# Kernel optimization log

Hardware: AMD Instinct MI355X
Metric: run time of the kernel (lower is better)

Reference implementation:

```python
import jax, jax.numpy as jnp
import numpy as np

N = 50000
E = 800000
IN_DIM = 128
HID = 64
HEADS = 4
OUT_DIM = 64
NEG_SLOPE = 0.2


def setup_inputs() -> dict:
    key = jax.random.key(0)
    ks = jax.random.split(key, 10)
    x = jax.random.normal(ks[0], (N, IN_DIM), dtype=jnp.float32)
    edge_index = jax.random.randint(ks[1], (2, E), 0, N, dtype=jnp.int64)
    s1 = 1.0 / np.sqrt(IN_DIM)
    s2 = 1.0 / np.sqrt(HEADS * HID)
    return {
        "x": x,
        "edge_index": edge_index,
        "W1": jax.random.normal(ks[2], (IN_DIM, HEADS * HID), dtype=jnp.float32) * s1,
        "a_src1": jax.random.normal(ks[3], (HEADS, HID), dtype=jnp.float32) * s2,
        "a_dst1": jax.random.normal(ks[4], (HEADS, HID), dtype=jnp.float32) * s2,
        "b1": jnp.zeros((HEADS * HID,), dtype=jnp.float32),
        "W2": jax.random.normal(ks[5], (HEADS * HID, OUT_DIM), dtype=jnp.float32) * s2,
        "a_src2": jax.random.normal(ks[6], (1, OUT_DIM), dtype=jnp.float32) * 0.125,
        "a_dst2": jax.random.normal(ks[7], (1, OUT_DIM), dtype=jnp.float32) * 0.125,
        "b2": jnp.zeros((OUT_DIM,), dtype=jnp.float32),
    }


def gat_layer(x, src, dst, W, a_src, a_dst, bias, heads, ch, concat):
    n = x.shape[0]
    h = (x @ W).reshape(n, heads, ch)                      # [N,H,C]
    asrc = jnp.einsum('nhc,hc->nh', h, a_src)              # [N,H]
    adst = jnp.einsum('nhc,hc->nh', h, a_dst)              # [N,H]
    e = asrc[src] + adst[dst]                              # [E',H]
    e = jnp.where(e > 0, e, NEG_SLOPE * e)                 # LeakyReLU(0.2)
    # segment softmax over incoming edges of each dst node
    m = jax.ops.segment_max(e, dst, num_segments=n)        # [N,H]
    m = jnp.where(jnp.isfinite(m), m, 0.0)
    ex = jnp.exp(e - m[dst])
    denom = jax.ops.segment_sum(ex, dst, num_segments=n)   # [N,H]
    alpha = ex / (denom[dst] + 1e-16)                      # [E',H]
    out = jax.ops.segment_sum(alpha[:, :, None] * h[src], dst, num_segments=n)  # [N,H,C]
    if concat:
        out = out.reshape(n, heads * ch)
    else:
        out = out.mean(axis=1)
    return out + bias


def reference(x, edge_index, W1, a_src1, a_dst1, b1, W2, a_src2, a_dst2, b2):
    n = x.shape[0]
    loops = jnp.arange(n, dtype=edge_index.dtype)
    src = jnp.concatenate([edge_index[0], loops])          # add self-loops (PyG default)
    dst = jnp.concatenate([edge_index[1], loops])
    h = gat_layer(x, src, dst, W1, a_src1, a_dst1, b1, HEADS, HID, True)
    h = jax.nn.elu(h)
    out = gat_layer(h, src, dst, W2, a_src2, a_dst2, b2, 1, OUT_DIM, False)
    return out
```

## Files before the change

### kernel.cpp

```cpp
#include <hip/hip_runtime.h>
#include <hip/hip_bf16.h>

#define NN 50000
#define EE 800000
#define IN_DIM 128
#define HH 256
#define HID 64
#define HEADS 4
#define OUT_DIM 64
#define SCAN_BLOCKS 196
#define G1_BLOCKS 782
#define AGG_BLOCKS 3125
#define TOTW (AGG_BLOCKS * 4)

static __device__ __forceinline__ unsigned short f2bf(float f) {
    unsigned int u = __float_as_uint(f);
    u += 0x7fffu + ((u >> 16) & 1u);
    return (unsigned short)(u >> 16);
}
static __device__ __forceinline__ float bf2f(unsigned short h) {
    return __uint_as_float(((unsigned int)h) << 16);
}


__global__ void hist_kernel(const int* __restrict__ ei, int* __restrict__ deg) {
    int e = blockIdx.x * 256 + threadIdx.x;
    atomicAdd(&deg[ei[EE + e]], 1);
}

__global__ __launch_bounds__(256) void block_scan_kernel(
    const int* __restrict__ deg, int* __restrict__ local_scan,
    int* __restrict__ block_sum) {
    __shared__ int tmp[256];
    int t = threadIdx.x, i = blockIdx.x * 256 + t;
    int v = (i < NN) ? deg[i] : 0;
    tmp[t] = v;
    __syncthreads();
    for (int d = 1; d < 256; d <<= 1) {
        int u = (t >= d) ? tmp[t - d] : 0;
        __syncthreads();
        tmp[t] += u;
        __syncthreads();
    }
    if (i < NN) local_scan[i] = tmp[t] - v;
    if (t == 255) block_sum[blockIdx.x] = tmp[255];
}

__global__ __launch_bounds__(256) void scan_sums_kernel(int* __restrict__ block_sum) {
    __shared__ int tmp[256];
    int t = threadIdx.x;
    int v = (t < SCAN_BLOCKS) ? block_sum[t] : 0;
    tmp[t] = v;
    __syncthreads();
    for (int d = 1; d < 256; d <<= 1) {
        int u = (t >= d) ? tmp[t - d] : 0;
        __syncthreads();
        tmp[t] += u;
        __syncthreads();
    }
    if (t < SCAN_BLOCKS) block_sum[t] = tmp[t] - v;
}

__global__ __launch_bounds__(256) void finalize_kernel(
    const int* __restrict__ local_scan, const int* __restrict__ block_sum,
    int* __restrict__ row_ptr, int* __restrict__ cursor) {
    int i = blockIdx.x * 256 + threadIdx.x;
    if (i < NN) {
        int v = local_scan[i] + block_sum[blockIdx.x];
        row_ptr[i] = v; cursor[i] = v;
    }
    if (i == 0) row_ptr[NN] = EE;
}

__global__ void scatter_kernel(const int* __restrict__ ei, int* __restrict__ cursor,
                               int* __restrict__ edge_src) {
    int e = blockIdx.x * 256 + threadIdx.x;
    int d = ei[EE + e];
    int pos = atomicAdd(&cursor[d], 1);
    edge_src[pos] = ei[e];
}


__global__ __launch_bounds__(256) void gemm1_kernel(
    const float* __restrict__ x, const float* __restrict__ W1,
    const float* __restrict__ a_src1, const float* __restrict__ a_dst1,
    unsigned short* __restrict__ h1, float* __restrict__ asrc1, float* __restrict__ adst1) {
    __shared__ __align__(16) float xs[64][IN_DIM];
    int t = threadIdx.x;
    int row0 = blockIdx.x * 64;
    #pragma unroll
    for (int j = 0; j < 8; j++) {
        int idx = t + j * 256;
        int r = idx >> 5, k4 = (idx & 31) * 4;
        int rr = row0 + r; if (rr >= NN) rr = NN - 1;
        *reinterpret_cast<float4*>(&xs[r][k4]) =
            *reinterpret_cast<const float4*>(&x[(size_t)rr * IN_DIM + k4]);
    }
    __syncthreads();
    int lane = t & 63, wid = t >> 6;
    float4 acc[16];
    #pragma unroll
    for (int r = 0; r < 16; r++) acc[r] = make_float4(0.f, 0.f, 0.f, 0.f);
    const float* wbase = W1 + lane * 4;
    float4 w0 = *reinterpret_cast<const float4*>(&wbase[0 * HH]);
    float4 w1 = *reinterpret_cast<const float4*>(&wbase[1 * HH]);
    float4 w2 = *reinterpret_cast<const float4*>(&wbase[2 * HH]);
    float4 w3 = *reinterpret_cast<const float4*>(&wbase[3 * HH]);
    for (int k = 0; k < IN_DIM; k += 4) {
        int kn = (k + 4) & 127;
        float4 nw0 = *reinterpret_cast<const float4*>(&wbase[(kn + 0) * HH]);
        float4 nw1 = *reinterpret_cast<const float4*>(&wbase[(kn + 1) * HH]);
        float4 nw2 = *reinterpret_cast<const float4*>(&wbase[(kn + 2) * HH]);
        float4 nw3 = *reinterpret_cast<const float4*>(&wbase[(kn + 3) * HH]);
        #pragma unroll
        for (int r = 0; r < 16; r++) {
            float4 xv = *reinterpret_cast<const float4*>(&xs[wid * 16 + r][k]);
            acc[r].x = fmaf(xv.x, w0.x, acc[r].x); acc[r].y = fmaf(xv.x, w0.y, acc[r].y);
            acc[r].z = fmaf(xv.x, w0.z, acc[r].z); acc[r].w = fmaf(xv.x, w0.w, acc[r].w);
            acc[r].x = fmaf(xv.y, w1.x, acc[r].x); acc[r].y = fmaf(xv.y, w1.y, acc[r].y);
            acc[r].z = fmaf(xv.y, w1.z, acc[r].z); acc[r].w = fmaf(xv.y, w1.w, acc[r].w);
            acc[r].x = fmaf(xv.z, w2.x, acc[r].x); acc[r].y = fmaf(xv.z, w2.y, acc[r].y);
            acc[r].z = fmaf(xv.z, w2.z, acc[r].z); acc[r].w = fmaf(xv.z, w2.w, acc[r].w);
            acc[r].x = fmaf(xv.w, w3.x, acc[r].x); acc[r].y = fmaf(xv.w, w3.y, acc[r].y);
            acc[r].z = fmaf(xv.w, w3.z, acc[r].z); acc[r].w = fmaf(xv.w, w3.w, acc[r].w);
        }
        w0 = nw0; w1 = nw1; w2 = nw2; w3 = nw3;
    }
    float4 asv = *reinterpret_cast<const float4*>(&a_src1[lane * 4]);
    float4 adv = *reinterpret_cast<const float4*>(&a_dst1[lane * 4]);
    int head = lane >> 4;
    #pragma unroll
    for (int r = 0; r < 16; r++) {
        int row = row0 + wid * 16 + r;
        bool ok = row < NN;
        if (ok) {
            ushort4 hv;
            hv.x = f2bf(acc[r].x); hv.y = f2bf(acc[r].y);
            hv.z = f2bf(acc[r].z); hv.w = f2bf(acc[r].w);
            *reinterpret_cast<ushort4*>(&h1[(size_t)row * HH + lane * 4]) = hv;
        }
        float vs = acc[r].x * asv.x + acc[r].y * asv.y + acc[r].z * asv.z + acc[r].w * asv.w;
        float vd = acc[r].x * adv.x + acc[r].y * adv.y + acc[r].z * adv.z + acc[r].w * adv.w;
        #pragma unroll
        for (int o = 1; o < 16; o <<= 1) { vs += __shfl_xor(vs, o); vd += __shfl_xor(vd, o); }
        if (ok && (lane & 15) == 0) {
            asrc1[row * HEADS + head] = vs;
            adst1[row * HEADS + head] = vd;
        }
    }
}


__global__ __launch_bounds__(256) void agg1_kernel(
    const int* __restrict__ row_ptr, const int* __restrict__ edge_src,
    const unsigned short* __restrict__ h1, const float* __restrict__ asrc1,
    const float* __restrict__ adst1, const float* __restrict__ b1,
    unsigned short* __restrict__ x2) {
    int wid = threadIdx.x >> 6, lane = threadIdx.x & 63;
    int gw = blockIdx.x * 4 + wid;
    int head = lane >> 4;
    unsigned cb = lane * 4;
    const unsigned short* h1l = h1 + cb;
    const float* asl = asrc1 + head;
    float4 bv = *reinterpret_cast<const float4*>(&b1[cb]);
    for (int node = gw; node < NN; node += TOTW) {
        float ad = adst1[node * HEADS + head];
        int beg = row_ptr[node], end = row_ptr[node + 1];
        float denom = 0.f;
        float ax = 0.f, ay = 0.f, az = 0.f, aw = 0.f;
        int s0 = (beg < end) ? edge_src[beg] : node;
        int s1 = (beg + 1 < end) ? edge_src[beg + 1] : node;
        int s2 = (beg + 2 < end) ? edge_src[beg + 2] : node;
        float e0 = asl[(unsigned)s0 * HEADS];
        float e1 = asl[(unsigned)s1 * HEADS];
        float e2 = asl[(unsigned)s2 * HEADS];
        ushort4 h0 = *reinterpret_cast<const ushort4*>(&h1l[(unsigned)s0 * HH]);
        ushort4 h1v = *reinterpret_cast<const ushort4*>(&h1l[(unsigned)s1 * HH]);
        ushort4 h2v = *reinterpret_cast<const ushort4*>(&h1l[(unsigned)s2 * HH]);
        for (int i = beg; i <= end; i++) {
            int j = i + 3;
            int s3 = (j < end) ? edge_src[j] : node;
            float e3 = asl[(unsigned)s3 * HEADS];
            ushort4 h3 = *reinterpret_cast<const ushort4*>(&h1l[(unsigned)s3 * HH]);
            float e = e0 + ad;
            e = fmaxf(e, 0.2f * e);
            float ex = __expf(e);
            denom += ex;
            ax = fmaf(ex, bf2f(h0.x), ax); ay = fmaf(ex, bf2f(h0.y), ay);
            az = fmaf(ex, bf2f(h0.z), az); aw = fmaf(ex, bf2f(h0.w), aw);
            e0 = e1; h0 = h1v;
            e1 = e2; h1v = h2v;
            e2 = e3; h2v = h3;
        }
        float inv = 1.0f / (denom + 1e-16f);
        float v0 = ax * inv + bv.x;
        float v1 = ay * inv + bv.y;
        float v2 = az * inv + bv.z;
        float v3 = aw * inv + bv.w;
        v0 = v0 > 0.f ? v0 : (__expf(v0) - 1.f);
        v1 = v1 > 0.f ? v1 : (__expf(v1) - 1.f);
        v2 = v2 > 0.f ? v2 : (__expf(v2) - 1.f);
        v3 = v3 > 0.f ? v3 : (__expf(v3) - 1.f);
        ushort4 o;
        o.x = f2bf(v0); o.y = f2bf(v1); o.z = f2bf(v2); o.w = f2bf(v3);
        *reinterpret_cast<ushort4*>(&x2[(size_t)node * HH + cb]) = o;
    }
}


__global__ __launch_bounds__(256) void gemm2_kernel(
    const unsigned short* __restrict__ x2, const float* __restrict__ W2,
    const float* __restrict__ a_src2, const float* __restrict__ a_dst2,
    unsigned short* __restrict__ h2, float* __restrict__ asrc2, float* __restrict__ adst2) {
    __shared__ __align__(16) float xs[32][HH];
    int t = threadIdx.x;
    int row0 = blockIdx.x * 32;
    #pragma unroll
    for (int j = 0; j < 8; j++) {
        int idx = t + j * 256;
        int r = idx >> 6, k4 = (idx & 63) * 4;
        int rr = row0 + r; if (rr >= NN) rr = NN - 1;
        ushort4 uv = *reinterpret_cast<const ushort4*>(&x2[(size_t)rr * HH + k4]);
        float4 fv;
        fv.x = bf2f(uv.x); fv.y = bf2f(uv.y); fv.z = bf2f(uv.z); fv.w = bf2f(uv.w);
        *reinterpret_cast<float4*>(&xs[r][k4]) = fv;
    }
    __syncthreads();
    int c = t & 63, wid = t >> 6;
    float acc[8];
    #pragma unroll
    for (int r = 0; r < 8; r++) acc[r] = 0.f;
    const float* wbase = W2 + c;
    float w0 = wbase[0 * OUT_DIM];
    float w1 = wbase[1 * OUT_DIM];
    float w2 = wbase[2 * OUT_DIM];
    float w3 = wbase[3 * OUT_DIM];
    for (int k = 0; k < HH; k += 4) {
        int kn = (k + 4) & 255;
        float nw0 = wbase[(kn + 0) * OUT_DIM];
        float nw1 = wbase[(kn + 1) * OUT_DIM];
        float nw2 = wbase[(kn + 2) * OUT_DIM];
        float nw3 = wbase[(kn + 3) * OUT_DIM];
        #pragma unroll
        for (int r = 0; r < 8; r++) {
            float4 xv = *reinterpret_cast<const float4*>(&xs[wid * 8 + r][k]);
            acc[r] = fmaf(xv.x, w0, acc[r]);
            acc[r] = fmaf(xv.y, w1, acc[r]);
            acc[r] = fmaf(xv.z, w2, acc[r]);
            acc[r] = fmaf(xv.w, w3, acc[r]);
        }
        w0 = nw0; w1 = nw1; w2 = nw2; w3 = nw3;
    }
    float as = a_src2[c], ad = a_dst2[c];
    #pragma unroll
    for (int r = 0; r < 8; r++) {
        int row = row0 + wid * 8 + r;
        bool ok = row < NN;
        if (ok) h2[(size_t)row * OUT_DIM + c] = f2bf(acc[r]);
        float vs = acc[r] * as, vd = acc[r] * ad;
        #pragma unroll
        for (int o = 32; o > 0; o >>= 1) { vs += __shfl_xor(vs, o); vd += __shfl_xor(vd, o); }
        if (ok && c == 0) { asrc2[row] = vs; adst2[row] = vd; }
    }
}


__global__ __launch_bounds__(256) void agg2_kernel(
    const int* __restrict__ row_ptr, const int* __restrict__ edge_src,
    const unsigned short* __restrict__ h2, const float* __restrict__ asrc2,
    const float* __restrict__ adst2, const float* __restrict__ b2,
    float* __restrict__ out) {
    int wid = threadIdx.x >> 6, lane = threadIdx.x & 63;
    int gw = blockIdx.x * 4 + wid;
    const unsigned short* h2l = h2 + lane;
    float bl = b2[lane];
    for (int node = gw; node < NN; node += TOTW) {
        float ad = adst2[node];
        int beg = row_ptr[node], end = row_ptr[node + 1];
        float denom = 0.f, acc = 0.f;
        int s0 = (beg < end) ? edge_src[beg] : node;
        int s1 = (beg + 1 < end) ? edge_src[beg + 1] : node;
        int s2 = (beg + 2 < end) ? edge_src[beg + 2] : node;
        float e0 = asrc2[s0], e1 = asrc2[s1], e2 = asrc2[s2];
        unsigned short h0 = h2l[(unsigned)s0 * OUT_DIM];
        unsigned short h1v = h2l[(unsigned)s1 * OUT_DIM];
        unsigned short h2v = h2l[(unsigned)s2 * OUT_DIM];
        for (int i = beg; i <= end; i++) {
            int j = i + 3;
            int s3 = (j < end) ? edge_src[j] : node;
            float e3 = asrc2[s3];
            unsigned short h3 = h2l[(unsigned)s3 * OUT_DIM];
            float e = e0 + ad;
            e = fmaxf(e, 0.2f * e);
            float ex = __expf(e);
            denom += ex;
            acc = fmaf(ex, bf2f(h0), acc);
            e0 = e1; h0 = h1v;
            e1 = e2; h1v = h2v;
            e2 = e3; h2v = h3;
        }
        out[(size_t)node * OUT_DIM + lane] = acc / (denom + 1e-16f) + bl;
    }
}


extern "C" void kernel_launch(void* const* d_in, const int* in_sizes, int n_in,
                              void* d_out, int out_size, void* d_ws, size_t ws_size,
                              hipStream_t stream) {
    const float* x   = (const float*)d_in[0];
    const int*   ei  = (const int*)d_in[1];
    const float* W1  = (const float*)d_in[2];
    const float* as1 = (const float*)d_in[3];
    const float* ad1 = (const float*)d_in[4];
    const float* b1  = (const float*)d_in[5];
    const float* W2  = (const float*)d_in[6];
    const float* as2 = (const float*)d_in[7];
    const float* ad2 = (const float*)d_in[8];
    const float* b2  = (const float*)d_in[9];
    float* out = (float*)d_out;

    char* ws = (char*)d_ws;
    size_t off = 0;
    auto alloc = [&](size_t bytes) -> void* {
        void* p = ws + off;
        off += (bytes + 255) & ~(size_t)255;
        return p;
    };
    unsigned short* h1 = (unsigned short*)alloc((size_t)NN * HH * 2);
    unsigned short* x2 = (unsigned short*)alloc((size_t)NN * HH * 2);
    unsigned short* h2 = (unsigned short*)alloc((size_t)NN * OUT_DIM * 2);
    float* asrc1  = (float*)alloc((size_t)NN * HEADS * 4);
    float* adst1  = (float*)alloc((size_t)NN * HEADS * 4);
    float* asrc2  = (float*)alloc((size_t)NN * 4);
    float* adst2  = (float*)alloc((size_t)NN * 4);
    int*   deg    = (int*)alloc((size_t)NN * 4);
    int*   row_ptr= (int*)alloc((size_t)(NN + 1) * 4);
    int*   cursor = (int*)alloc((size_t)NN * 4);
    int*   edge_src=(int*)alloc((size_t)EE * 4);
    int*   local_scan = (int*)alloc((size_t)NN * 4);
    int*   block_sum  = (int*)alloc((size_t)SCAN_BLOCKS * 4);

    hipMemsetAsync(deg, 0, (size_t)NN * 4, stream);
    hist_kernel<<<EE / 256, 256, 0, stream>>>(ei, deg);
    block_scan_kernel<<<SCAN_BLOCKS, 256, 0, stream>>>(deg, local_scan, block_sum);
    scan_sums_kernel<<<1, 256, 0, stream>>>(block_sum);
    finalize_kernel<<<SCAN_BLOCKS, 256, 0, stream>>>(local_scan, block_sum, row_ptr, cursor);
    gemm1_kernel<<<G1_BLOCKS, 256, 0, stream>>>(x, W1, as1, ad1, h1, asrc1, adst1);
    scatter_kernel<<<EE / 256, 256, 0, stream>>>(ei, cursor, edge_src);

    agg1_kernel<<<AGG_BLOCKS, 256, 0, stream>>>(row_ptr, edge_src, h1, asrc1, adst1, b1, x2);
    gemm2_kernel<<<(NN + 31) / 32, 256, 0, stream>>>(x2, W2, as2, ad2, h2, asrc2, adst2);
    agg2_kernel<<<AGG_BLOCKS, 256, 0, stream>>>(row_ptr, edge_src, h2, asrc2, adst2, b2, out);
}
```

Baseline: 418.1 us.

## Use bf16 MFMA for layer-1 GEMM and fold attention vectors into W1

Replaces the FP32 FMA layer-1 GEMM with a bf16 MFMA 16x16x32 kernel that reads a bf16 copy of x and a transposed bf16 W1. The per-head attention logits are now computed in a separate conversion pass as x·(W1·a) using a precomputed 128x8 projection, so the GEMM kernel only writes h1. This adds a single-block prep kernel and an extra pass over x, plus bf16 rounding of the inputs. The gemm2 weight prefetch is also simplified to direct loads.

After: 454.6 us. 8.7% more time.

```diff
diff --git a/kernel.cpp b/kernel.cpp
--- a/kernel.cpp
+++ b/kernel.cpp
@@ -9,7 +9,9 @@
 #define HEADS 4
 #define OUT_DIM 64
 #define SCAN_BLOCKS 196
-#define G1_BLOCKS 782
+#define G1M_BLOCKS 782
+#define XCVT_BLOCKS 1563
+#define XCVT_TOTW (XCVT_BLOCKS * 4)
 #define AGG_BLOCKS 3125
 #define TOTW (AGG_BLOCKS * 4)
 
@@ -21,6 +23,9 @@
 static __device__ __forceinline__ float bf2f(unsigned short h) {
     return __uint_as_float(((unsigned int)h) << 16);
 }
+
+typedef __attribute__((ext_vector_type(8))) __bf16 bf16x8;
+typedef __attribute__((ext_vector_type(4))) float f32x4;
 
 
 __global__ void hist_kernel(const int* __restrict__ ei, int* __restrict__ deg) {
@@ -81,71 +86,87 @@
 }
 
 
-__global__ __launch_bounds__(256) void gemm1_kernel(
-    const float* __restrict__ x, const float* __restrict__ W1,
-    const float* __restrict__ a_src1, const float* __restrict__ a_dst1,
-    unsigned short* __restrict__ h1, float* __restrict__ asrc1, float* __restrict__ adst1) {
-    __shared__ __align__(16) float xs[64][IN_DIM];
+__global__ __launch_bounds__(256) void u_prep_kernel(
+    const float* __restrict__ W1, const float* __restrict__ as1,
+    const float* __restrict__ ad1, float* __restrict__ u1,
+    unsigned short* __restrict__ W1T) {
     int t = threadIdx.x;
-    int row0 = blockIdx.x * 64;
+    for (int idx = t; idx < 1024; idx += 256) {
+        int k = idx >> 3, j = idx & 7;
+        int hd = j & 3;
+        const float* av = ((j >= 4) ? ad1 : as1) + hd * 64;
+        const float* wr = W1 + k * HH + hd * 64;
+        float s = 0.f;
+        for (int c = 0; c < 64; c++) s += wr[c] * av[c];
+        u1[idx] = s;
+    }
+    for (int idx = t; idx < HH * IN_DIM; idx += 256) {
+        int c = idx >> 7, k = idx & 127;
+        W1T[idx] = f2bf(W1[k * HH + c]);
+    }
+}
+
+
+__global__ __launch_bounds__(256) void xcvt_kernel(
+    const float* __restrict__ x, const float* __restrict__ u1,
+    unsigned short* __restrict__ x_bf, float* __restrict__ asrc1,
+    float* __restrict__ adst1) {
+    int t = threadIdx.x, lane = t & 63, wid = t >> 6;
+    int gw = blockIdx.x * 4 + wid;
+    float uA[8], uB[8];
     #pragma unroll
     for (int j = 0; j < 8; j++) {
-        int idx = t + j * 256;
-        int r = idx >> 5, k4 = (idx & 31) * 4;
-        int rr = row0 + r; if (rr >= NN) rr = NN - 1;
-        *reinterpret_cast<float4*>(&xs[r][k4]) =
-            *reinterpret_cast<const float4*>(&x[(size_t)rr * IN_DIM + k4]);
-    }
-    __syncthreads();
-    int lane = t & 63, wid = t >> 6;
-    float4 acc[16];
-    #pragma unroll
-    for (int r = 0; r < 16; r++) acc[r] = make_float4(0.f, 0.f, 0.f, 0.f);
-    const float* wbase = W1 + lane * 4;
-    float4 w0 = *reinterpret_cast<const float4*>(&wbase[0 * HH]);
-    float4 w1 = *reinterpret_cast<const float4*>(&wbase[1 * HH]);
-    float4 w2 = *reinterpret_cast<const float4*>(&wbase[2 * HH]);
-    float4 w3 = *reinterpret_cast<const float4*>(&wbase[3 * HH]);
-    for (int k = 0; k < IN_DIM; k += 4) {
-        int kn = (k + 4) & 127;
-        float4 nw0 = *reinterpret_cast<const float4*>(&wbase[(kn + 0) * HH]);
-        float4 nw1 = *reinterpret_cast<const float4*>(&wbase[(kn + 1) * HH]);
-        float4 nw2 = *reinterpret_cast<const float4*>(&wbase[(kn + 2) * HH]);
-        float4 nw3 = *reinterpret_cast<const float4*>(&wbase[(kn + 3) * HH]);
-        #pragma unroll
-        for (int r = 0; r < 16; r++) {
-            float4 xv = *reinterpret_cast<const float4*>(&xs[wid * 16 + r][k]);
-            acc[r].x = fmaf(xv.x, w0.x, acc[r].x); acc[r].y = fmaf(xv.x, w0.y, acc[r].y);
-            acc[r].z = fmaf(xv.x, w0.z, acc[r].z); acc[r].w = fmaf(xv.x, w0.w, acc[r].w);
-            acc[r].x = fmaf(xv.y, w1.x, acc[r].x); acc[r].y = fmaf(xv.y, w1.y, acc[r].y);
-            acc[r].z = fmaf(xv.y, w1.z, acc[r].z); acc[r].w = fmaf(xv.y, w1.w, acc[r].w);
-            acc[r].x = fmaf(xv.z, w2.x, acc[r].x); acc[r].y = fmaf(xv.z, w2.y, acc[r].y);
-            acc[r].z = fmaf(xv.z, w2.z, acc[r].z); acc[r].w = fmaf(xv.z, w2.w, acc[r].w);
-            acc[r].x = fmaf(xv.w, w3.x, acc[r].x); acc[r].y = fmaf(xv.w, w3.y, acc[r].y);
-            acc[r].z = fmaf(xv.w, w3.z, acc[r].z); acc[r].w = fmaf(xv.w, w3.w, acc[r].w);
-        }
-        w0 = nw0; w1 = nw1; w2 = nw2; w3 = nw3;
-    }
-    float4 asv = *reinterpret_cast<const float4*>(&a_src1[lane * 4]);
-    float4 adv = *reinterpret_cast<const float4*>(&a_dst1[lane * 4]);
-    int head = lane >> 4;
-    #pragma unroll
-    for (int r = 0; r < 16; r++) {
-        int row = row0 + wid * 16 + r;
-        bool ok = row < NN;
-        if (ok) {
-            ushort4 hv;
-            hv.x = f2bf(acc[r].x); hv.y = f2bf(acc[r].y);
-            hv.z = f2bf(acc[r].z); hv.w = f2bf(acc[r].w);
-            *reinterpret_cast<ushort4*>(&h1[(size_t)row * HH + lane * 4]) = hv;
-        }
-        float vs = acc[r].x * asv.x + acc[r].y * asv.y + acc[r].z * asv.z + acc[r].w * asv.w;
-        float vd = acc[r].x * adv.x + acc[r].y * adv.y + acc[r].z * adv.z + acc[r].w * adv.w;
-        #pragma unroll
-        for (int o = 1; o < 16; o <<= 1) { vs += __shfl_xor(vs, o); vd += __shfl_xor(vd, o); }
-        if (ok && (lane & 15) == 0) {
-            asrc1[row * HEADS + head] = vs;
-            adst1[row * HEADS + head] = vd;
+        uA[j] = u1[(2 * lane) * 8 + j];
+        uB[j] = u1[(2 * lane + 1) * 8 + j];
+    }
+    for (int row = gw; row < NN; row += XCVT_TOTW) {
+        float2 xv = *reinterpret_cast<const float2*>(&x[(size_t)row * IN_DIM + lane * 2]);
+        ushort2 o; o.x = f2bf(xv.x); o.y = f2bf(xv.y);
+        *reinterpret_cast<ushort2*>(&x_bf[(size_t)row * IN_DIM + lane * 2]) = o;
+        float p[8];
+        #pragma unroll
+        for (int j = 0; j < 8; j++) p[j] = xv.x * uA[j] + xv.y * uB[j];
+        #pragma unroll
+        for (int off = 32; off > 0; off >>= 1) {
+            #pragma unroll
+            for (int j = 0; j < 8; j++) p[j] += __shfl_xor(p[j], off);
+        }
+        if (lane == 0) {
+            #pragma unroll
+            for (int h = 0; h < 4; h++) {
+                asrc1[row * HEADS + h] = p[h];
+                adst1[row * HEADS + h] = p[4 + h];
+            }
+        }
+    }
+}
+
+
+__global__ __launch_bounds__(256) void gemm1_mfma_kernel(
+    const unsigned short* __restrict__ x_bf, const unsigned short* __restrict__ W1T,
+    unsigned short* __restrict__ h1) {
+    int t = threadIdx.x, lane = t & 63, wid = t >> 6;
+    int row0w = blockIdx.x * 64 + wid * 16;
+    int m = lane & 15, ko = lane >> 4;
+    int ar = row0w + m; if (ar >= NN) ar = NN - 1;
+    bf16x8 a[4];
+    #pragma unroll
+    for (int kb = 0; kb < 4; kb++)
+        a[kb] = *reinterpret_cast<const bf16x8*>(&x_bf[(size_t)ar * IN_DIM + kb * 32 + ko * 8]);
+    #pragma unroll
+    for (int ct = 0; ct < 16; ct++) {
+        f32x4 acc = {0.f, 0.f, 0.f, 0.f};
+        #pragma unroll
+        for (int kb = 0; kb < 4; kb++) {
+            bf16x8 b = *reinterpret_cast<const bf16x8*>(
+                &W1T[(ct * 16 + m) * IN_DIM + kb * 32 + ko * 8]);
+            acc = __builtin_amdgcn_mfma_f32_16x16x32_bf16(a[kb], b, acc, 0, 0, 0);
+        }
+        int col = ct * 16 + m;
+        #pragma unroll
+        for (int r = 0; r < 4; r++) {
+            int row = row0w + ko * 4 + r;
+            if (row < NN) h1[(size_t)row * HH + col] = f2bf(acc[r]);
         }
     }
 }
@@ -230,17 +251,11 @@
     float acc[8];
     #pragma unroll
     for (int r = 0; r < 8; r++) acc[r] = 0.f;
-    const float* wbase = W2 + c;
-    float w0 = wbase[0 * OUT_DIM];
-    float w1 = wbase[1 * OUT_DIM];
-    float w2 = wbase[2 * OUT_DIM];
-    float w3 = wbase[3 * OUT_DIM];
     for (int k = 0; k < HH; k += 4) {
-        int kn = (k + 4) & 255;
-        float nw0 = wbase[(kn + 0) * OUT_DIM];
-        float nw1 = wbase[(kn + 1) * OUT_DIM];
-        float nw2 = wbase[(kn + 2) * OUT_DIM];
-        float nw3 = wbase[(kn + 3) * OUT_DIM];
+        float w0 = W2[(k + 0) * OUT_DIM + c];
+        float w1 = W2[(k + 1) * OUT_DIM + c];
+        float w2 = W2[(k + 2) * OUT_DIM + c];
+        float w3 = W2[(k + 3) * OUT_DIM + c];
         #pragma unroll
         for (int r = 0; r < 8; r++) {
             float4 xv = *reinterpret_cast<const float4*>(&xs[wid * 8 + r][k]);
@@ -249,7 +264,6 @@
             acc[r] = fmaf(xv.z, w2, acc[r]);
             acc[r] = fmaf(xv.w, w3, acc[r]);
         }
-        w0 = nw0; w1 = nw1; w2 = nw2; w3 = nw3;
     }
     float as = a_src2[c], ad = a_dst2[c];
     #pragma unroll
@@ -326,9 +340,12 @@
         off += (bytes + 255) & ~(size_t)255;
         return p;
     };
-    unsigned short* h1 = (unsigned short*)alloc((size_t)NN * HH * 2);
-    unsigned short* x2 = (unsigned short*)alloc((size_t)NN * HH * 2);
-    unsigned short* h2 = (unsigned short*)alloc((size_t)NN * OUT_DIM * 2);
+    unsigned short* h1  = (unsigned short*)alloc((size_t)NN * HH * 2);
+    unsigned short* x2  = (unsigned short*)alloc((size_t)NN * HH * 2);
+    unsigned short* h2  = (unsigned short*)alloc((size_t)NN * OUT_DIM * 2);
+    unsigned short* x_bf= (unsigned short*)alloc((size_t)NN * IN_DIM * 2);
+    unsigned short* W1T = (unsigned short*)alloc((size_t)HH * IN_DIM * 2);
+    float* u1     = (float*)alloc((size_t)IN_DIM * 8 * 4);
     float* asrc1  = (float*)alloc((size_t)NN * HEADS * 4);
     float* adst1  = (float*)alloc((size_t)NN * HEADS * 4);
     float* asrc2  = (float*)alloc((size_t)NN * 4);
@@ -341,11 +358,13 @@
     int*   block_sum  = (int*)alloc((size_t)SCAN_BLOCKS * 4);
 
     hipMemsetAsync(deg, 0, (size_t)NN * 4, stream);
+    u_prep_kernel<<<1, 256, 0, stream>>>(W1, as1, ad1, u1, W1T);
+    xcvt_kernel<<<XCVT_BLOCKS, 256, 0, stream>>>(x, u1, x_bf, asrc1, adst1);
     hist_kernel<<<EE / 256, 256, 0, stream>>>(ei, deg);
     block_scan_kernel<<<SCAN_BLOCKS, 256, 0, stream>>>(deg, local_scan, block_sum);
     scan_sums_kernel<<<1, 256, 0, stream>>>(block_sum);
     finalize_kernel<<<SCAN_BLOCKS, 256, 0, stream>>>(local_scan, block_sum, row_ptr, cursor);
-    gemm1_kernel<<<G1_BLOCKS, 256, 0, stream>>>(x, W1, as1, ad1, h1, asrc1, adst1);
+    gemm1_mfma_kernel<<<G1M_BLOCKS, 256, 0, stream>>>(x_bf, W1T, h1);
     scatter_kernel<<<EE / 256, 256, 0, stream>>>(ei, cursor, edge_src);
 
     agg1_kernel<<<AGG_BLOCKS, 256, 0, stream>>>(row_ptr, edge_src, h1, asrc1, adst1, b1, x2);
```
